# Performance work log

Hardware: AMD Instinct MI355X
Metric: run time of the kernel (lower is better)

The kernel has to match this reference:

```python
import jax, jax.numpy as jnp
import numpy as np

NEAR, FAR = 0.05, 6.0
STEPSIZE = 0.5
ALPHA_INIT = 1e-6
XYZ_MIN = np.array([-1.0, -1.0, -1.0], np.float32)
XYZ_MAX = np.array([1.0, 1.0, 1.0], np.float32)
WORLD = (160, 160, 160)
VOXEL_SIZE = 2.0 / 160.0  # ((prod span)/num_voxels)^(1/3)
N_SAMPLES = int(np.linalg.norm(np.array(WORLD) + 1) / STEPSIZE) + 1  # 558
ACT_SHIFT = float(np.log(1.0 / (1.0 - ALPHA_INIT) - 1.0))


def setup_inputs() -> dict:
    key = jax.random.key(0)
    k1, k2, k3, k4, k5, k6, k7 = jax.random.split(key, 7)
    rays_o = (jax.random.uniform(k1, (8192, 3), jnp.float32) - 0.5) * 1.2  # inside bbox
    rd = jax.random.normal(k2, (8192, 3), jnp.float32)
    rays_d = rd / jnp.linalg.norm(rd, axis=-1, keepdims=True)
    jitter = jax.random.uniform(k3, (8192, 1), jnp.float32)
    em_modes = jax.random.randint(k4, (8192,), 0, 2, jnp.int32)
    density = jax.random.normal(k5, (1, 160, 160, 160), jnp.float32) * 0.1
    off_color = jax.random.normal(k6, (3, 160, 160, 160), jnp.float32) * 0.1
    emo_color = jax.random.normal(k7, (3, 160, 160, 160), jnp.float32) * 0.1
    return {"rays_o": rays_o, "rays_d": rays_d, "jitter": jitter, "em_modes": em_modes,
            "density": density, "off_color": off_color, "emo_color": emo_color}


def grid_sampler(pts, grid):
    """Trilinear interp, align_corners=True, zero padding. grid [C,Nx,Ny,Nz], pts [...,3] -> [...,C]."""
    C = grid.shape[0]
    sizes = np.array(grid.shape[1:], np.int32)
    lead = pts.shape[:-1]
    t = (pts.reshape(-1, 3) - XYZ_MIN) / (XYZ_MAX - XYZ_MIN)
    idx = t * (jnp.asarray(sizes, pts.dtype) - 1)  # voxel-space coords
    i0 = jnp.floor(idx).astype(jnp.int32)
    f = idx - i0.astype(pts.dtype)
    out = jnp.zeros((i0.shape[0], C), grid.dtype)
    for corner in range(8):
        off = np.array([(corner >> 2) & 1, (corner >> 1) & 1, corner & 1], np.int32)
        ci = i0 + off  # [N,3]
        w = jnp.prod(jnp.where(off[None, :] == 1, f, 1.0 - f), axis=-1)  # [N]
        valid = jnp.all((ci >= 0) & (ci < sizes[None, :]), axis=-1)
        cc = jnp.clip(ci, 0, sizes[None, :] - 1)
        vals = grid[:, cc[:, 0], cc[:, 1], cc[:, 2]].T  # [N,C]
        out = out + (w * valid)[:, None] * vals
    return out.reshape(*lead, C)


def sample_ray(rays_o, rays_d, jitter):
    vec = jnp.where(rays_d == 0, 1e-6, rays_d)
    rate_a = (XYZ_MAX - rays_o) / vec
    rate_b = (XYZ_MIN - rays_o) / vec
    t_min = jnp.clip(jnp.minimum(rate_a, rate_b).max(-1), NEAR, FAR)
    t_max = jnp.clip(jnp.maximum(rate_a, rate_b).min(-1), NEAR, FAR)
    mask_out = t_max <= t_min  # [R]
    rng = jnp.arange(N_SAMPLES, dtype=rays_o.dtype)[None, :] + jitter  # [R,S]
    step = STEPSIZE * VOXEL_SIZE * rng
    interpx = t_min[:, None] + step / jnp.linalg.norm(rays_d, axis=-1, keepdims=True)
    rays_pts = rays_o[:, None, :] + rays_d[:, None, :] * interpx[..., None]  # [R,S,3]
    mask_out = mask_out[:, None] | ((rays_pts < XYZ_MIN) | (rays_pts > XYZ_MAX)).any(-1)
    return rays_pts, mask_out


def reference(rays_o, rays_d, jitter, em_modes, density, off_color, emo_color):
    rays_pts, mask_out = sample_ray(rays_o, rays_d, jitter)
    dens = grid_sampler(rays_pts, density)[..., 0]  # [R,S]
    alpha_all = 1.0 - jnp.exp(-jax.nn.softplus(dens + ACT_SHIFT) * STEPSIZE)
    alpha = jnp.where(mask_out, 0.0, alpha_all)
    p = jnp.clip(1.0 - alpha, 1e-10, None)
    alphainv_cum = jnp.concatenate([jnp.ones_like(p[..., :1]), jnp.cumprod(p, -1)], -1)  # [R,S+1]
    weights = alpha * alphainv_cum[..., :-1]
    on_mask = (em_modes == 1)[:, None, None]
    emo = jax.nn.sigmoid(grid_sampler(rays_pts, emo_color))
    off = jax.nn.sigmoid(grid_sampler(rays_pts, off_color))
    rgb = jnp.where(on_mask, emo, 0.0) + off  # [R,S,3]
    rgb_marched = (weights[..., None] * rgb).sum(-2)  # [R,3]
    return (alphainv_cum, weights, alphainv_cum[..., -1:], rgb, rgb_marched)
```

## Files before the change

### kernel.cpp

```cpp
#include <hip/hip_runtime.h>
#include <math.h>


namespace {
constexpr int   kR   = 8192;
constexpr int   kS   = 558;
constexpr int   kG   = 160;
constexpr int   kG2  = kG * kG;
constexpr int   kG3  = kG * kG * kG;
constexpr float kNear = 0.05f;
constexpr float kFar  = 6.0f;
constexpr float kStepWorld = 0.5f * (2.0f / 160.0f);
constexpr float kActShift = (float)-13.815509557963774;
constexpr size_t kPackedBytes = (size_t)kG3 * 16;
}

__device__ __forceinline__ float sigmoidf_(float x) {
  return 1.0f / (1.0f + expf(-x));
}
__device__ __forceinline__ float bf_lo(unsigned int u) {
  union { unsigned int i; float f; } x; x.i = u << 16; return x.f;
}
__device__ __forceinline__ float bf_hi(unsigned int u) {
  union { unsigned int i; float f; } x; x.i = u & 0xffff0000u; return x.f;
}
__device__ __forceinline__ unsigned short f2bf(float f) {
  union { float f; unsigned int i; } x; x.f = f;
  unsigned int lsb = (x.i >> 16) & 1u;
  return (unsigned short)((x.i + 0x7fffu + lsb) >> 16);
}

__global__ __launch_bounds__(256) void repack_grids(
    const float* __restrict__ density,
    const float* __restrict__ off_c,
    const float* __restrict__ emo_c,
    uint4* __restrict__ packed)
{
  const int v = blockIdx.x * blockDim.x + threadIdx.x;
  if (v >= kG3) return;
  const unsigned int d  = f2bf(density[v]);
  const unsigned int f0 = f2bf(off_c[v]);
  const unsigned int f1 = f2bf(off_c[v + kG3]);
  const unsigned int f2 = f2bf(off_c[v + 2 * kG3]);
  const unsigned int e0 = f2bf(emo_c[v]);
  const unsigned int e1 = f2bf(emo_c[v + kG3]);
  const unsigned int e2 = f2bf(emo_c[v + 2 * kG3]);
  uint4 q;
  q.x = d  | (f0 << 16);
  q.y = f1 | (f2 << 16);
  q.z = e0 | (e1 << 16);
  q.w = e2;
  packed[v] = q;
}

__global__ __launch_bounds__(256) void dvgo_fwd(
    const float* __restrict__ rays_o,
    const float* __restrict__ rays_d,
    const float* __restrict__ jitter,
    const int*   __restrict__ em_modes,
    const uint2* __restrict__ packed2,
    float* __restrict__ out)
{
  const int tid  = blockIdx.x * blockDim.x + threadIdx.x;
  const int ray  = tid >> 6;
  const int lane = tid & 63;
  if (ray >= kR) return;

  const float ox = rays_o[ray * 3 + 0];
  const float oy = rays_o[ray * 3 + 1];
  const float oz = rays_o[ray * 3 + 2];
  const float dx = rays_d[ray * 3 + 0];
  const float dy = rays_d[ray * 3 + 1];
  const float dz = rays_d[ray * 3 + 2];
  const float jit = jitter[ray];
  const bool  on  = (em_modes[ray] == 1);

  const float vx = (dx == 0.0f) ? 1e-6f : dx;
  const float vy = (dy == 0.0f) ? 1e-6f : dy;
  const float vz = (dz == 0.0f) ? 1e-6f : dz;
  const float rax = ( 1.0f - ox) / vx, rbx = (-1.0f - ox) / vx;
  const float ray_a = ( 1.0f - oy) / vy, rby = (-1.0f - oy) / vy;
  const float raz = ( 1.0f - oz) / vz, rbz = (-1.0f - oz) / vz;
  float tmin = fmaxf(fmaxf(fminf(rax, rbx), fminf(ray_a, rby)), fminf(raz, rbz));
  float tmax = fminf(fminf(fmaxf(rax, rbx), fmaxf(ray_a, rby)), fmaxf(raz, rbz));
  tmin = fminf(fmaxf(tmin, kNear), kFar);
  tmax = fminf(fmaxf(tmax, kNear), kFar);
  const bool  ray_out = (tmax <= tmin);
  const float dnorm = sqrtf(dx * dx + dy * dy + dz * dz);
  const float stepc = kStepWorld / dnorm;

  float* out_ainv = out;
  float* out_w    = out + (size_t)kR * (kS + 1);
  float* out_last = out_w + (size_t)kR * kS;
  float* out_rgb  = out_last + kR;
  float* out_rm   = out_rgb + (size_t)kR * kS * 3;

  if (lane == 0) out_ainv[(size_t)ray * (kS + 1)] = 1.0f;

  float carry = 1.0f;
  float accr = 0.0f, accg = 0.0f, accb = 0.0f;

  #pragma unroll 1
  for (int chunk = 0; chunk < (kS + 63) / 64; ++chunk) {
    const int  s      = chunk * 64 + lane;
    const bool active = (s < kS);

    const float t  = tmin + stepc * ((float)s + jit);
    const float px = fmaf(dx, t, ox);
    const float py = fmaf(dy, t, oy);
    const float pz = fmaf(dz, t, oz);
    const bool inb = (px >= -1.0f) & (px <= 1.0f) &
                     (py >= -1.0f) & (py <= 1.0f) &
                     (pz >= -1.0f) & (pz <= 1.0f);
    const bool masked = ray_out || !inb;

    const float fx = (px + 1.0f) * 0.5f * (float)(kG - 1);
    const float fy = (py + 1.0f) * 0.5f * (float)(kG - 1);
    const float fz = (pz + 1.0f) * 0.5f * (float)(kG - 1);
    const int ix = (int)floorf(fx);
    const int iy = (int)floorf(fy);
    const int iz = (int)floorf(fz);
    const float wx = fx - (float)ix;
    const float wy = fy - (float)iy;
    const float wz = fz - (float)iz;

    const float x0 = 1.0f - wx, y0 = 1.0f - wy, z0 = 1.0f - wz;
    const float wxy00 = x0 * y0, wxy01 = x0 * wy;
    const float wxy10 = wx * y0, wxy11 = wx * wy;
    float w8[8];
    w8[0] = wxy00 * z0; w8[1] = wxy00 * wz;
    w8[2] = wxy01 * z0; w8[3] = wxy01 * wz;
    w8[4] = wxy10 * z0; w8[5] = wxy10 * wz;
    w8[6] = wxy11 * z0; w8[7] = wxy11 * wz;

    float dsum = 0.0f;
    float o0 = 0.0f, o1 = 0.0f, o2 = 0.0f;
    float e0 = 0.0f, e1 = 0.0f, e2 = 0.0f;

    const bool interior = active &&
        (ix >= 0) && (ix < kG - 1) &&
        (iy >= 0) && (iy < kG - 1) &&
        (iz >= 0) && (iz < kG - 1);
    const bool any = active && !interior &&
        (ix >= -1) && (ix <= kG - 1) &&
        (iy >= -1) && (iy <= kG - 1) &&
        (iz >= -1) && (iz <= kG - 1);

    if (interior) {
      const int base = (ix * kG + iy) * kG + iz;
      #pragma unroll
      for (int c = 0; c < 8; ++c) {
        const int gi = base + ((c >> 2) & 1) * kG2 + ((c >> 1) & 1) * kG + (c & 1);
        const float w = w8[c];
        const uint2 qa = packed2[(size_t)gi * 2];
        dsum = fmaf(w, bf_lo(qa.x), dsum);
        o0   = fmaf(w, bf_hi(qa.x), o0);
        o1   = fmaf(w, bf_lo(qa.y), o1);
        o2   = fmaf(w, bf_hi(qa.y), o2);
        if (on) {
          const uint2 qb = packed2[(size_t)gi * 2 + 1];
          e0 = fmaf(w, bf_lo(qb.x), e0);
          e1 = fmaf(w, bf_hi(qb.x), e1);
          e2 = fmaf(w, bf_lo(qb.y), e2);
        }
      }
    } else if (any) {
      #pragma unroll
      for (int c = 0; c < 8; ++c) {
        const int cx = ix + ((c >> 2) & 1);
        const int cy = iy + ((c >> 1) & 1);
        const int cz = iz + (c & 1);
        const bool valid = ((unsigned)cx < (unsigned)kG) &
                           ((unsigned)cy < (unsigned)kG) &
                           ((unsigned)cz < (unsigned)kG);
        const float wv = valid ? w8[c] : 0.0f;
        const int gx = min(max(cx, 0), kG - 1);
        const int gy = min(max(cy, 0), kG - 1);
        const int gz = min(max(cz, 0), kG - 1);
        const int gi = (gx * kG + gy) * kG + gz;
        const uint2 qa = packed2[(size_t)gi * 2];
        dsum = fmaf(wv, bf_lo(qa.x), dsum);
        o0   = fmaf(wv, bf_hi(qa.x), o0);
        o1   = fmaf(wv, bf_lo(qa.y), o1);
        o2   = fmaf(wv, bf_hi(qa.y), o2);
        if (on) {
          const uint2 qb = packed2[(size_t)gi * 2 + 1];
          e0 = fmaf(wv, bf_lo(qb.x), e0);
          e1 = fmaf(wv, bf_hi(qb.x), e1);
          e2 = fmaf(wv, bf_lo(qb.y), e2);
        }
      }
    }

    float alpha = 0.0f;
    if (active && !masked) {
      const float x  = dsum + kActShift;
      const float sp = fmaxf(x, 0.0f) + log1pf(expf(-fabsf(x)));
      alpha = 1.0f - expf(-sp * 0.5f);
    }
    float p = fmaxf(1.0f - alpha, 1e-10f);
    if (!active) p = 1.0f;

    float incl = p;
    #pragma unroll
    for (int o = 1; o < 64; o <<= 1) {
      const float n = __shfl_up(incl, o, 64);
      if (lane >= o) incl *= n;
    }
    float excl = __shfl_up(incl, 1, 64);
    if (lane == 0) excl = 1.0f;
    const float ainv_prev = carry * excl;
    const float ainv_next = carry * incl;
    const float wgt = alpha * ainv_prev;
    carry *= __shfl(incl, 63, 64);

    float rr = sigmoidf_(o0);
    float gg = sigmoidf_(o1);
    float bb = sigmoidf_(o2);
    if (on) {
      rr += sigmoidf_(e0);
      gg += sigmoidf_(e1);
      bb += sigmoidf_(e2);
    }

    if (active) {
      out_ainv[(size_t)ray * (kS + 1) + s + 1] = ainv_next;
      out_w[(size_t)ray * kS + s] = wgt;
      const size_t rb = ((size_t)ray * kS + s) * 3;
      out_rgb[rb + 0] = rr;
      out_rgb[rb + 1] = gg;
      out_rgb[rb + 2] = bb;
      accr = fmaf(wgt, rr, accr);
      accg = fmaf(wgt, gg, accg);
      accb = fmaf(wgt, bb, accb);
    }
  }

  #pragma unroll
  for (int o = 32; o > 0; o >>= 1) {
    accr += __shfl_xor(accr, o, 64);
    accg += __shfl_xor(accg, o, 64);
    accb += __shfl_xor(accb, o, 64);
  }
  if (lane == 0) {
    out_last[ray] = carry;
    out_rm[(size_t)ray * 3 + 0] = accr;
    out_rm[(size_t)ray * 3 + 1] = accg;
    out_rm[(size_t)ray * 3 + 2] = accb;
  }
}

extern "C" void kernel_launch(void* const* d_in, const int* in_sizes, int n_in,
                              void* d_out, int out_size, void* d_ws, size_t ws_size,
                              hipStream_t stream) {
  const float* rays_o  = (const float*)d_in[0];
  const float* rays_d  = (const float*)d_in[1];
  const float* jitter  = (const float*)d_in[2];
  const int*   em      = (const int*)d_in[3];
  const float* density = (const float*)d_in[4];
  const float* off_c   = (const float*)d_in[5];
  const float* emo_c   = (const float*)d_in[6];
  float* out = (float*)d_out;

  uint4* packed = (uint4*)d_ws;
  (void)ws_size;

  hipLaunchKernelGGL(repack_grids, dim3((kG3 + 255) / 256), dim3(256), 0,
                     stream, density, off_c, emo_c, packed);

  const int threads = 256;
  const int blocks  = (kR * 64) / threads;
  hipLaunchKernelGGL(dvgo_fwd, dim3(blocks), dim3(threads), 0, stream,
                     rays_o, rays_d, jitter, em, (const uint2*)packed, out);
}
```

Before: 264.5 us.

## Skip grid sampling after ray exits, split packed grids, use fast intrinsics

The main loop now uses a wave ballot to detect when no sample of a ray can reach the grid. From that point it stops sampling and writes constant outputs: carry, zero weight, and sigmoid(0) colors. The grids are repacked into two separate 8-byte arrays (density+off, emo), so off-mode rays touch a compact array, and the repack kernel reads float4 vectors. Softplus/alpha is reduced algebraically to p = rsqrt(1+exp(x)), and divisions, exps and sqrts use hardware approximate intrinsics, which adds some rounding risk. bf_hi drops its mask, leaving low bits as small noise in the value.

```diff
diff --git a/kernel.cpp b/kernel.cpp
--- a/kernel.cpp
+++ b/kernel.cpp
@@ -11,46 +11,62 @@
 constexpr float kNear = 0.05f;
 constexpr float kFar  = 6.0f;
 constexpr float kStepWorld = 0.5f * (2.0f / 160.0f);
-constexpr float kActShift = (float)-13.815509557963774;
-constexpr size_t kPackedBytes = (size_t)kG3 * 16;
-}
-
+constexpr float kActShift = -13.815509557963774f;
+constexpr float kLog2e = 1.4426950408889634f;
+}
+
+__device__ __forceinline__ float fexp(float x) {
+  return __builtin_amdgcn_exp2f(x * kLog2e);
+}
 __device__ __forceinline__ float sigmoidf_(float x) {
-  return 1.0f / (1.0f + expf(-x));
+  return __builtin_amdgcn_rcpf(1.0f + fexp(-x));
 }
 __device__ __forceinline__ float bf_lo(unsigned int u) {
   union { unsigned int i; float f; } x; x.i = u << 16; return x.f;
 }
 __device__ __forceinline__ float bf_hi(unsigned int u) {
-  union { unsigned int i; float f; } x; x.i = u & 0xffff0000u; return x.f;
-}
-__device__ __forceinline__ unsigned short f2bf(float f) {
+  union { unsigned int i; float f; } x; x.i = u; return x.f;
+}
+__device__ __forceinline__ unsigned int f2bf(float f) {
   union { float f; unsigned int i; } x; x.f = f;
   unsigned int lsb = (x.i >> 16) & 1u;
-  return (unsigned short)((x.i + 0x7fffu + lsb) >> 16);
+  return (x.i + 0x7fffu + lsb) >> 16;
 }
 
 __global__ __launch_bounds__(256) void repack_grids(
-    const float* __restrict__ density,
-    const float* __restrict__ off_c,
-    const float* __restrict__ emo_c,
-    uint4* __restrict__ packed)
+    const float4* __restrict__ dens4,
+    const float4* __restrict__ off4,
+    const float4* __restrict__ emo4,
+    uint2* __restrict__ arrA,
+    uint2* __restrict__ arrB)
 {
-  const int v = blockIdx.x * blockDim.x + threadIdx.x;
-  if (v >= kG3) return;
-  const unsigned int d  = f2bf(density[v]);
-  const unsigned int f0 = f2bf(off_c[v]);
-  const unsigned int f1 = f2bf(off_c[v + kG3]);
-  const unsigned int f2 = f2bf(off_c[v + 2 * kG3]);
-  const unsigned int e0 = f2bf(emo_c[v]);
-  const unsigned int e1 = f2bf(emo_c[v + kG3]);
-  const unsigned int e2 = f2bf(emo_c[v + 2 * kG3]);
-  uint4 q;
-  q.x = d  | (f0 << 16);
-  q.y = f1 | (f2 << 16);
-  q.z = e0 | (e1 << 16);
-  q.w = e2;
-  packed[v] = q;
+  const int v4 = blockIdx.x * blockDim.x + threadIdx.x;
+  constexpr int kQ = kG3 / 4;
+  if (v4 >= kQ) return;
+  const float4 d  = dens4[v4];
+  const float4 f0 = off4[v4];
+  const float4 f1 = off4[v4 + kQ];
+  const float4 f2 = off4[v4 + 2 * kQ];
+  const float4 e0 = emo4[v4];
+  const float4 e1 = emo4[v4 + kQ];
+  const float4 e2 = emo4[v4 + 2 * kQ];
+  const float dv[4]  = {d.x, d.y, d.z, d.w};
+  const float f0v[4] = {f0.x, f0.y, f0.z, f0.w};
+  const float f1v[4] = {f1.x, f1.y, f1.z, f1.w};
+  const float f2v[4] = {f2.x, f2.y, f2.z, f2.w};
+  const float e0v[4] = {e0.x, e0.y, e0.z, e0.w};
+  const float e1v[4] = {e1.x, e1.y, e1.z, e1.w};
+  const float e2v[4] = {e2.x, e2.y, e2.z, e2.w};
+  #pragma unroll
+  for (int j = 0; j < 4; ++j) {
+    uint2 a, b;
+    a.x = f2bf(dv[j])  | (f2bf(f0v[j]) << 16);
+    a.y = f2bf(f1v[j]) | (f2bf(f2v[j]) << 16);
+    b.x = f2bf(e0v[j]) | (f2bf(e1v[j]) << 16);
+    b.y = f2bf(e2v[j]);
+    arrA[4 * v4 + j] = a;
+    arrB[4 * v4 + j] = b;
+  }
 }
 
 __global__ __launch_bounds__(256) void dvgo_fwd(
@@ -58,7 +74,8 @@
     const float* __restrict__ rays_d,
     const float* __restrict__ jitter,
     const int*   __restrict__ em_modes,
-    const uint2* __restrict__ packed2,
+    const uint2* __restrict__ arrA,
+    const uint2* __restrict__ arrB,
     float* __restrict__ out)
 {
   const int tid  = blockIdx.x * blockDim.x + threadIdx.x;
@@ -78,16 +95,19 @@
   const float vx = (dx == 0.0f) ? 1e-6f : dx;
   const float vy = (dy == 0.0f) ? 1e-6f : dy;
   const float vz = (dz == 0.0f) ? 1e-6f : dz;
-  const float rax = ( 1.0f - ox) / vx, rbx = (-1.0f - ox) / vx;
-  const float ray_a = ( 1.0f - oy) / vy, rby = (-1.0f - oy) / vy;
-  const float raz = ( 1.0f - oz) / vz, rbz = (-1.0f - oz) / vz;
+  const float ivx = __builtin_amdgcn_rcpf(vx);
+  const float ivy = __builtin_amdgcn_rcpf(vy);
+  const float ivz = __builtin_amdgcn_rcpf(vz);
+  const float rax = ( 1.0f - ox) * ivx, rbx = (-1.0f - ox) * ivx;
+  const float ray_a = ( 1.0f - oy) * ivy, rby = (-1.0f - oy) * ivy;
+  const float raz = ( 1.0f - oz) * ivz, rbz = (-1.0f - oz) * ivz;
   float tmin = fmaxf(fmaxf(fminf(rax, rbx), fminf(ray_a, rby)), fminf(raz, rbz));
   float tmax = fminf(fminf(fmaxf(rax, rbx), fmaxf(ray_a, rby)), fmaxf(raz, rbz));
   tmin = fminf(fmaxf(tmin, kNear), kFar);
   tmax = fminf(fmaxf(tmax, kNear), kFar);
   const bool  ray_out = (tmax <= tmin);
-  const float dnorm = sqrtf(dx * dx + dy * dy + dz * dz);
-  const float stepc = kStepWorld / dnorm;
+  const float stepc = kStepWorld *
+      __builtin_amdgcn_rsqf(dx * dx + dy * dy + dz * dz);
 
   float* out_ainv = out;
   float* out_w    = out + (size_t)kR * (kS + 1);
@@ -97,142 +117,159 @@
 
   if (lane == 0) out_ainv[(size_t)ray * (kS + 1)] = 1.0f;
 
+  const float c_base = on ? 1.0f : 0.5f;
+
   float carry = 1.0f;
   float accr = 0.0f, accg = 0.0f, accb = 0.0f;
+  bool dead = false;
 
   #pragma unroll 1
   for (int chunk = 0; chunk < (kS + 63) / 64; ++chunk) {
     const int  s      = chunk * 64 + lane;
     const bool active = (s < kS);
 
-    const float t  = tmin + stepc * ((float)s + jit);
-    const float px = fmaf(dx, t, ox);
-    const float py = fmaf(dy, t, oy);
-    const float pz = fmaf(dz, t, oz);
-    const bool inb = (px >= -1.0f) & (px <= 1.0f) &
-                     (py >= -1.0f) & (py <= 1.0f) &
-                     (pz >= -1.0f) & (pz <= 1.0f);
-    const bool masked = ray_out || !inb;
-
-    const float fx = (px + 1.0f) * 0.5f * (float)(kG - 1);
-    const float fy = (py + 1.0f) * 0.5f * (float)(kG - 1);
-    const float fz = (pz + 1.0f) * 0.5f * (float)(kG - 1);
-    const int ix = (int)floorf(fx);
-    const int iy = (int)floorf(fy);
-    const int iz = (int)floorf(fz);
-    const float wx = fx - (float)ix;
-    const float wy = fy - (float)iy;
-    const float wz = fz - (float)iz;
-
-    const float x0 = 1.0f - wx, y0 = 1.0f - wy, z0 = 1.0f - wz;
-    const float wxy00 = x0 * y0, wxy01 = x0 * wy;
-    const float wxy10 = wx * y0, wxy11 = wx * wy;
-    float w8[8];
-    w8[0] = wxy00 * z0; w8[1] = wxy00 * wz;
-    w8[2] = wxy01 * z0; w8[3] = wxy01 * wz;
-    w8[4] = wxy10 * z0; w8[5] = wxy10 * wz;
-    w8[6] = wxy11 * z0; w8[7] = wxy11 * wz;
-
-    float dsum = 0.0f;
-    float o0 = 0.0f, o1 = 0.0f, o2 = 0.0f;
-    float e0 = 0.0f, e1 = 0.0f, e2 = 0.0f;
-
-    const bool interior = active &&
-        (ix >= 0) && (ix < kG - 1) &&
-        (iy >= 0) && (iy < kG - 1) &&
-        (iz >= 0) && (iz < kG - 1);
-    const bool any = active && !interior &&
-        (ix >= -1) && (ix <= kG - 1) &&
-        (iy >= -1) && (iy <= kG - 1) &&
-        (iz >= -1) && (iz <= kG - 1);
-
-    if (interior) {
-      const int base = (ix * kG + iy) * kG + iz;
-      #pragma unroll
-      for (int c = 0; c < 8; ++c) {
-        const int gi = base + ((c >> 2) & 1) * kG2 + ((c >> 1) & 1) * kG + (c & 1);
-        const float w = w8[c];
-        const uint2 qa = packed2[(size_t)gi * 2];
-        dsum = fmaf(w, bf_lo(qa.x), dsum);
-        o0   = fmaf(w, bf_hi(qa.x), o0);
-        o1   = fmaf(w, bf_lo(qa.y), o1);
-        o2   = fmaf(w, bf_hi(qa.y), o2);
+    if (!dead) {
+      const float t  = tmin + stepc * ((float)s + jit);
+      const float px = fmaf(dx, t, ox);
+      const float py = fmaf(dy, t, oy);
+      const float pz = fmaf(dz, t, oz);
+      const bool inb = (px >= -1.0f) & (px <= 1.0f) &
+                       (py >= -1.0f) & (py <= 1.0f) &
+                       (pz >= -1.0f) & (pz <= 1.0f);
+      const bool masked = ray_out || !inb;
+
+      const float fx = (px + 1.0f) * 0.5f * (float)(kG - 1);
+      const float fy = (py + 1.0f) * 0.5f * (float)(kG - 1);
+      const float fz = (pz + 1.0f) * 0.5f * (float)(kG - 1);
+      const int ix = (int)floorf(fx);
+      const int iy = (int)floorf(fy);
+      const int iz = (int)floorf(fz);
+
+      const bool reach = active &&
+          (ix >= -1) && (ix <= kG - 1) &&
+          (iy >= -1) && (iy <= kG - 1) &&
+          (iz >= -1) && (iz <= kG - 1);
+      if (__ballot(reach) == 0ull) {
+        dead = true;
+      } else {
+        const float wx = fx - (float)ix;
+        const float wy = fy - (float)iy;
+        const float wz = fz - (float)iz;
+        const float x0 = 1.0f - wx, y0 = 1.0f - wy, z0 = 1.0f - wz;
+        const float wxy00 = x0 * y0, wxy01 = x0 * wy;
+        const float wxy10 = wx * y0, wxy11 = wx * wy;
+        float w8[8];
+        w8[0] = wxy00 * z0; w8[1] = wxy00 * wz;
+        w8[2] = wxy01 * z0; w8[3] = wxy01 * wz;
+        w8[4] = wxy10 * z0; w8[5] = wxy10 * wz;
+        w8[6] = wxy11 * z0; w8[7] = wxy11 * wz;
+
+        float dsum = 0.0f;
+        float o0 = 0.0f, o1 = 0.0f, o2 = 0.0f;
+        float e0 = 0.0f, e1 = 0.0f, e2 = 0.0f;
+
+        const bool interior = active &&
+            (ix >= 0) && (ix < kG - 1) &&
+            (iy >= 0) && (iy < kG - 1) &&
+            (iz >= 0) && (iz < kG - 1);
+
+        if (interior) {
+          const int base = (ix * kG + iy) * kG + iz;
+          #pragma unroll
+          for (int c = 0; c < 8; ++c) {
+            const int gi = base + ((c >> 2) & 1) * kG2 + ((c >> 1) & 1) * kG + (c & 1);
+            const float w = w8[c];
+            const uint2 qa = arrA[gi];
+            dsum = fmaf(w, bf_lo(qa.x), dsum);
+            o0   = fmaf(w, bf_hi(qa.x), o0);
+            o1   = fmaf(w, bf_lo(qa.y), o1);
+            o2   = fmaf(w, bf_hi(qa.y), o2);
+            if (on) {
+              const uint2 qb = arrB[gi];
+              e0 = fmaf(w, bf_lo(qb.x), e0);
+              e1 = fmaf(w, bf_hi(qb.x), e1);
+              e2 = fmaf(w, bf_lo(qb.y), e2);
+            }
+          }
+        } else if (reach) {
+          #pragma unroll
+          for (int c = 0; c < 8; ++c) {
+            const int cx = ix + ((c >> 2) & 1);
+            const int cy = iy + ((c >> 1) & 1);
+            const int cz = iz + (c & 1);
+            const bool valid = ((unsigned)cx < (unsigned)kG) &
+                               ((unsigned)cy < (unsigned)kG) &
+                               ((unsigned)cz < (unsigned)kG);
+            const float wv = valid ? w8[c] : 0.0f;
+            const int gx = min(max(cx, 0), kG - 1);
+            const int gy = min(max(cy, 0), kG - 1);
+            const int gz = min(max(cz, 0), kG - 1);
+            const int gi = (gx * kG + gy) * kG + gz;
+            const uint2 qa = arrA[gi];
+            dsum = fmaf(wv, bf_lo(qa.x), dsum);
+            o0   = fmaf(wv, bf_hi(qa.x), o0);
+            o1   = fmaf(wv, bf_lo(qa.y), o1);
+            o2   = fmaf(wv, bf_hi(qa.y), o2);
+            if (on) {
+              const uint2 qb = arrB[gi];
+              e0 = fmaf(wv, bf_lo(qb.x), e0);
+              e1 = fmaf(wv, bf_hi(qb.x), e1);
+              e2 = fmaf(wv, bf_lo(qb.y), e2);
+            }
+          }
+        }
+
+        float p = 1.0f;
+        if (active && !masked) {
+          const float ex = fexp(dsum + kActShift);
+          p = fmaxf(__builtin_amdgcn_rsqf(1.0f + ex), 1e-10f);
+        }
+        const float alpha = 1.0f - p;
+
+        float incl = p;
+        #pragma unroll
+        for (int o = 1; o < 64; o <<= 1) {
+          const float n = __shfl_up(incl, o, 64);
+          if (lane >= o) incl *= n;
+        }
+        float excl = __shfl_up(incl, 1, 64);
+        if (lane == 0) excl = 1.0f;
+        const float ainv_prev = carry * excl;
+        const float ainv_next = carry * incl;
+        const float wgt = alpha * ainv_prev;
+        carry *= __shfl(incl, 63, 64);
+
+        float rr = sigmoidf_(o0);
+        float gg = sigmoidf_(o1);
+        float bb = sigmoidf_(o2);
         if (on) {
-          const uint2 qb = packed2[(size_t)gi * 2 + 1];
-          e0 = fmaf(w, bf_lo(qb.x), e0);
-          e1 = fmaf(w, bf_hi(qb.x), e1);
-          e2 = fmaf(w, bf_lo(qb.y), e2);
-        }
-      }
-    } else if (any) {
-      #pragma unroll
-      for (int c = 0; c < 8; ++c) {
-        const int cx = ix + ((c >> 2) & 1);
-        const int cy = iy + ((c >> 1) & 1);
-        const int cz = iz + (c & 1);
-        const bool valid = ((unsigned)cx < (unsigned)kG) &
-                           ((unsigned)cy < (unsigned)kG) &
-                           ((unsigned)cz < (unsigned)kG);
-        const float wv = valid ? w8[c] : 0.0f;
-        const int gx = min(max(cx, 0), kG - 1);
-        const int gy = min(max(cy, 0), kG - 1);
-        const int gz = min(max(cz, 0), kG - 1);
-        const int gi = (gx * kG + gy) * kG + gz;
-        const uint2 qa = packed2[(size_t)gi * 2];
-        dsum = fmaf(wv, bf_lo(qa.x), dsum);
-        o0   = fmaf(wv, bf_hi(qa.x), o0);
-        o1   = fmaf(wv, bf_lo(qa.y), o1);
-        o2   = fmaf(wv, bf_hi(qa.y), o2);
-        if (on) {
-          const uint2 qb = packed2[(size_t)gi * 2 + 1];
-          e0 = fmaf(wv, bf_lo(qb.x), e0);
-          e1 = fmaf(wv, bf_hi(qb.x), e1);
-          e2 = fmaf(wv, bf_lo(qb.y), e2);
-        }
+          rr += sigmoidf_(e0);
+          gg += sigmoidf_(e1);
+          bb += sigmoidf_(e2);
+        }
+
+        if (active) {
+          out_ainv[(size_t)ray * (kS + 1) + s + 1] = ainv_next;
+          out_w[(size_t)ray * kS + s] = wgt;
+          const size_t rb = ((size_t)ray * kS + s) * 3;
+          out_rgb[rb + 0] = rr;
+          out_rgb[rb + 1] = gg;
+          out_rgb[rb + 2] = bb;
+          accr = fmaf(wgt, rr, accr);
+          accg = fmaf(wgt, gg, accg);
+          accb = fmaf(wgt, bb, accb);
+        }
+        continue;
       }
     }
 
-    float alpha = 0.0f;
-    if (active && !masked) {
-      const float x  = dsum + kActShift;
-      const float sp = fmaxf(x, 0.0f) + log1pf(expf(-fabsf(x)));
-      alpha = 1.0f - expf(-sp * 0.5f);
-    }
-    float p = fmaxf(1.0f - alpha, 1e-10f);
-    if (!active) p = 1.0f;
-
-    float incl = p;
-    #pragma unroll
-    for (int o = 1; o < 64; o <<= 1) {
-      const float n = __shfl_up(incl, o, 64);
-      if (lane >= o) incl *= n;
-    }
-    float excl = __shfl_up(incl, 1, 64);
-    if (lane == 0) excl = 1.0f;
-    const float ainv_prev = carry * excl;
-    const float ainv_next = carry * incl;
-    const float wgt = alpha * ainv_prev;
-    carry *= __shfl(incl, 63, 64);
-
-    float rr = sigmoidf_(o0);
-    float gg = sigmoidf_(o1);
-    float bb = sigmoidf_(o2);
-    if (on) {
-      rr += sigmoidf_(e0);
-      gg += sigmoidf_(e1);
-      bb += sigmoidf_(e2);
-    }
-
     if (active) {
-      out_ainv[(size_t)ray * (kS + 1) + s + 1] = ainv_next;
-      out_w[(size_t)ray * kS + s] = wgt;
+      out_ainv[(size_t)ray * (kS + 1) + s + 1] = carry;
+      out_w[(size_t)ray * kS + s] = 0.0f;
       const size_t rb = ((size_t)ray * kS + s) * 3;
-      out_rgb[rb + 0] = rr;
-      out_rgb[rb + 1] = gg;
-      out_rgb[rb + 2] = bb;
-      accr = fmaf(wgt, rr, accr);
-      accg = fmaf(wgt, gg, accg);
-      accb = fmaf(wgt, bb, accb);
+      out_rgb[rb + 0] = c_base;
+      out_rgb[rb + 1] = c_base;
+      out_rgb[rb + 2] = c_base;
     }
   }
 
@@ -262,14 +299,17 @@
   const float* emo_c   = (const float*)d_in[6];
   float* out = (float*)d_out;
 
-  uint4* packed = (uint4*)d_ws;
+  uint2* arrA = (uint2*)d_ws;
+  uint2* arrB = arrA + kG3;
   (void)ws_size;
 
-  hipLaunchKernelGGL(repack_grids, dim3((kG3 + 255) / 256), dim3(256), 0,
-                     stream, density, off_c, emo_c, packed);
+  constexpr int kQ = kG3 / 4;
+  hipLaunchKernelGGL(repack_grids, dim3((kQ + 255) / 256), dim3(256), 0,
+                     stream, (const float4*)density, (const float4*)off_c,
+                     (const float4*)emo_c, arrA, arrB);
 
   const int threads = 256;
   const int blocks  = (kR * 64) / threads;
   hipLaunchKernelGGL(dvgo_fwd, dim3(blocks), dim3(threads), 0, stream,
-                     rays_o, rays_d, jitter, em, (const uint2*)packed, out);
-}
+                     rays_o, rays_d, jitter, em, arrA, arrB, out);
+}
```

Result: slower. 273.7 us (+3.5%).
